# Performance work log

Hardware: AMD Instinct MI355X
Metric: run time of the kernel (lower is better)

Reference implementation:

```python
import jax, jax.numpy as jnp
import numpy as np

N_NODES = 100000
N_EDGES = 1600000
K = 3  # TAGConv default hops


def _make_lin(key, out_dim, in_dim):
    # K+1 bias-free linears (stacked) + one shared output bias, per PyG TAGConv
    kw, = jax.random.split(key, 1)
    scale = 1.0 / np.sqrt(in_dim)
    W = jax.random.uniform(kw, (K + 1, out_dim, in_dim), jnp.float32, -scale, scale)
    b = jnp.zeros((out_dim,), jnp.float32)
    return W, b


def setup_inputs() -> dict:
    key = jax.random.key(0)
    ks = jax.random.split(key, 6)
    x = jax.random.normal(ks[0], (N_NODES, 128), jnp.float32)
    edge_index = jax.random.randint(ks[1], (2, N_EDGES), 0, N_NODES, jnp.int64)
    W1, b1 = _make_lin(ks[2], 128, 128)
    W2, b2 = _make_lin(ks[3], 64, 128)
    W3, b3 = _make_lin(ks[4], 16, 64)
    return {"x": x, "edge_index": edge_index, "W1": W1, "b1": b1,
            "W2": W2, "b2": b2, "W3": W3, "b3": b3}


def _tagconv(x, row, col, norm, W, b, n):
    # out = sum_k lin_k(A_norm^k x) + b ; message x_j*norm gathered at col
    out = jnp.einsum('nd,od->no', x, W[0])
    h = x
    for k in range(1, W.shape[0]):
        h = jax.ops.segment_sum(norm[:, None] * h[row], col, num_segments=n)
        out = out + jnp.einsum('nd,od->no', h, W[k])
    return out + b


def _dropout(x, key, p=0.5):
    keep = jax.random.bernoulli(key, 1.0 - p, x.shape)
    return jnp.where(keep, x / (1.0 - p), 0.0)


def reference(x, edge_index, W1, b1, W2, b2, W3, b3):
    n = x.shape[0]
    row, col = edge_index[0], edge_index[1]
    # gcn_norm without self-loops (TAGConv default)
    deg = jax.ops.segment_sum(jnp.ones(row.shape[0], x.dtype), col, num_segments=n)
    dis = jnp.where(deg > 0, 1.0 / jnp.sqrt(jnp.where(deg > 0, deg, 1.0)), 0.0)
    norm = dis[row] * dis[col]

    dk1, dk2 = jax.random.split(jax.random.key(42))
    h = _tagconv(x, row, col, norm, W1, b1, n)
    h = _dropout(h, dk1)
    h = _tagconv(h, row, col, norm, W2, b2, n)
    h = jax.nn.elu(h)
    h = _dropout(h, dk2)
    h = _tagconv(h, row, col, norm, W3, b3, n)
    return h
```

## Files before the change

### kernel.cpp

```cpp
#include <hip/hip_runtime.h>
#include <stdint.h>
#include <math.h>

#define N_NODES 100000
#define N_EDGES 1600000

typedef __bf16 bf16_t;
typedef __attribute__((ext_vector_type(4))) __bf16 bf16x4;
typedef __attribute__((ext_vector_type(8))) __bf16 bf16x8;
typedef __attribute__((ext_vector_type(4))) float f32x4;

__device__ __forceinline__ f32x4 mfma16(bf16x8 a, bf16x8 b, f32x4 c) {
  return __builtin_amdgcn_mfma_f32_16x16x32_bf16(a, b, c, 0, 0, 0);
}

__device__ __host__ __forceinline__ uint32_t rotl32(uint32_t v, int d) {
  return (v << d) | (v >> (32 - d));
}

__device__ __host__ __forceinline__ void threefry2x32(uint32_t k0, uint32_t k1,
                                                      uint32_t x0, uint32_t x1,
                                                      uint32_t& o0, uint32_t& o1) {
  uint32_t ks0 = k0, ks1 = k1, ks2 = k0 ^ k1 ^ 0x1BD11BDAu;
  x0 += ks0; x1 += ks1;
#define TF_R(r) { x0 += x1; x1 = rotl32(x1, r); x1 ^= x0; }
  TF_R(13) TF_R(15) TF_R(26) TF_R(6)
  x0 += ks1; x1 += ks2 + 1u;
  TF_R(17) TF_R(29) TF_R(16) TF_R(24)
  x0 += ks2; x1 += ks0 + 2u;
  TF_R(13) TF_R(15) TF_R(26) TF_R(6)
  x0 += ks0; x1 += ks1 + 3u;
  TF_R(17) TF_R(29) TF_R(16) TF_R(24)
  x0 += ks1; x1 += ks2 + 4u;
  TF_R(13) TF_R(15) TF_R(26) TF_R(6)
  x0 += ks2; x1 += ks0 + 5u;
#undef TF_R
  o0 = x0; o1 = x1;
}

__device__ __forceinline__ float drop_scale(uint32_t idx, uint32_t k0, uint32_t k1) {
  uint32_t o0, o1;
  threefry2x32(k0, k1, 0u, idx, o0, o1);
  uint32_t bits = o0 ^ o1;
  float u = __uint_as_float((bits >> 9) | 0x3f800000u) - 1.0f;
  return (u < 0.5f) ? 2.0f : 0.0f;
}

__global__ __launch_bounds__(256) void detect_kernel(const int* __restrict__ ei,
                                                     int* __restrict__ found_nonzero) {
  int idx = blockIdx.x * 256 + threadIdx.x;
  size_t j = (size_t)idx * 781;
  if (ei[2 * j + 1] != 0) atomicOr(found_nonzero, 1);
}

__device__ __forceinline__ int edge_row(const int* ei, bool i32, int e) {
  return i32 ? ei[e] : ei[2 * (size_t)e];
}
__device__ __forceinline__ int edge_col(const int* ei, bool i32, int e) {
  return i32 ? ei[N_EDGES + e] : ei[2 * ((size_t)N_EDGES + (size_t)e)];
}

#define BKT_SHIFT 8
#define NBKT 391
#define BKT_CAP 6144
#define EPB 8192
#define NBLK 196
#define SCAN_M (NBKT * NBLK)

__global__ __launch_bounds__(256) void hist_kernel(const int* __restrict__ ei,
                                                   const int* __restrict__ flag,
                                                   int* __restrict__ hist) {
  __shared__ int h[NBKT];
  const int t = threadIdx.x, blk = blockIdx.x;
  for (int i = t; i < NBKT; i += 256) h[i] = 0;
  __syncthreads();
  const bool i32 = *flag != 0;
  const int e0 = blk * EPB;
  for (int i = t; i < EPB; i += 256) {
    int e = e0 + i;
    if (e < N_EDGES) atomicAdd(&h[edge_col(ei, i32, e) >> BKT_SHIFT], 1);
  }
  __syncthreads();
  for (int i = t; i < NBKT; i += 256) hist[i * NBLK + blk] = h[i];
}

__global__ __launch_bounds__(256) void btot_kernel(const int* __restrict__ hist,
                                                   int* __restrict__ btot) {
  __shared__ int sh[256];
  const int b = blockIdx.x, t = threadIdx.x;
  int s = 0;
  for (int i = t; i < NBLK; i += 256) s += hist[b * NBLK + i];
  sh[t] = s;
  __syncthreads();
  for (int ofs = 128; ofs > 0; ofs >>= 1) {
    if (t < ofs) sh[t] += sh[t + ofs];
    __syncthreads();
  }
  if (t == 0) btot[b] = sh[0];
}

__global__ __launch_bounds__(512) void bbase_kernel(const int* __restrict__ btot,
                                                    int* __restrict__ bbase,
                                                    int* __restrict__ S) {
  __shared__ int sh[512];
  const int t = threadIdx.x;
  int v = (t < NBKT) ? btot[t] : 0;
  sh[t] = v;
  __syncthreads();
  for (int ofs = 1; ofs < 512; ofs <<= 1) {
    int u = (t >= ofs) ? sh[t - ofs] : 0;
    __syncthreads();
    sh[t] += u;
    __syncthreads();
  }
  if (t < NBKT) bbase[t] = sh[t] - v;
  if (t == 0) S[SCAN_M] = N_EDGES;
}

__global__ __launch_bounds__(256) void bscan2_kernel(const int* __restrict__ hist,
                                                     const int* __restrict__ bbase,
                                                     int* __restrict__ S) {
  __shared__ int sh[256];
  const int b = blockIdx.x, t = threadIdx.x;
  int v = (t < NBLK) ? hist[b * NBLK + t] : 0;
  sh[t] = v;
  __syncthreads();
  for (int ofs = 1; ofs < 256; ofs <<= 1) {
    int u = (t >= ofs) ? sh[t - ofs] : 0;
    __syncthreads();
    sh[t] += u;
    __syncthreads();
  }
  if (t < NBLK) S[b * NBLK + t] = bbase[b] + sh[t] - v;
}

__global__ __launch_bounds__(256) void binfill_kernel(const int* __restrict__ ei,
                                                      const int* __restrict__ flag,
                                                      const int* __restrict__ S,
                                                      int2* __restrict__ bins) {
  __shared__ int cur[NBKT];
  const int t = threadIdx.x, blk = blockIdx.x;
  for (int i = t; i < NBKT; i += 256) cur[i] = S[i * NBLK + blk];
  __syncthreads();
  const bool i32 = *flag != 0;
  const int e0 = blk * EPB;
  for (int i = t; i < EPB; i += 256) {
    int e = e0 + i;
    if (e < N_EDGES) {
      int r = edge_row(ei, i32, e);
      int c = edge_col(ei, i32, e);
      int p = atomicAdd(&cur[c >> BKT_SHIFT], 1);
      bins[p] = make_int2(r, c);
    }
  }
}

__global__ __launch_bounds__(512) void degdis_scatter_kernel(
    const int2* __restrict__ bins, const int* __restrict__ S,
    float* __restrict__ dis, int* __restrict__ rptr,
    uint32_t* __restrict__ erow) {
  __shared__ int h[256];
  __shared__ int sc[256];
  __shared__ int loff[256];
  __shared__ int lcur[256];
  __shared__ uint32_t reord[BKT_CAP];
  const int b = blockIdx.x, t = threadIdx.x;
  const int Bb = S[b * NBLK];
  const int Be = S[(b + 1) * NBLK];
  const int cnt = min(Be - Bb, BKT_CAP);
  if (t < 256) h[t] = 0;
  __syncthreads();
  for (int i = t; i < cnt; i += 512)
    atomicAdd(&h[bins[Bb + i].y & 255], 1);
  __syncthreads();
  if (t < 256) sc[t] = h[t];
  __syncthreads();
  for (int ofs = 1; ofs < 256; ofs <<= 1) {
    int u = 0;
    if (t >= ofs && t < 256) u = sc[t - ofs];
    __syncthreads();
    if (t < 256) sc[t] += u;
    __syncthreads();
  }
  const int c0 = b << BKT_SHIFT;
  if (t < 256) {
    loff[t] = sc[t] - h[t];
    lcur[t] = 0;
    if (c0 + t < N_NODES) {
      int d = h[t];
      dis[c0 + t] = (d > 0) ? (1.0f / sqrtf((float)d)) : 0.0f;
      rptr[c0 + t] = Bb + sc[t] - d;
    }
  }
  if (b == NBKT - 1 && t == 0) rptr[N_NODES] = N_EDGES;
  __syncthreads();
  for (int i = t; i < cnt; i += 512) {
    int2 rec = bins[Bb + i];
    int lc = rec.y & 255;
    int p = atomicAdd(&lcur[lc], 1);
    reord[loff[lc] + p] = (uint32_t)rec.x;
  }
  __syncthreads();
  for (int i = t; i < cnt; i += 512) erow[Bb + i] = reord[i];
}

__global__ __launch_bounds__(256) void wcvt_kernel(
    const float* __restrict__ W1, const float* __restrict__ W2,
    const float* __restrict__ W3,
    bf16_t* __restrict__ Wb1, bf16_t* __restrict__ Wb2,
    bf16_t* __restrict__ Wb3) {
  int i = blockIdx.x * 256 + threadIdx.x;
  if (i < 65536) Wb1[i] = (bf16_t)W1[i];
  if (i < 32768) Wb2[i] = (bf16_t)W2[i];
  if (i < 4096)  Wb3[i] = (bf16_t)W3[i];
}

template <int DIN, int LOG_DOUT, int NCH, bool YB, bool AHL>
__global__ __launch_bounds__(256) void matmul_mfma_kernel(
    const void* __restrict__ hA, const void* __restrict__ hAlo,
    const bf16_t* __restrict__ Wb, const float* __restrict__ bias,
    float* __restrict__ y0, void* __restrict__ y1,
    void* __restrict__ y2, void* __restrict__ y3) {
  constexpr int LDK = DIN + 8;
  constexpr int DOUT = 1 << LOG_DOUT;
  constexpr int KI = DIN / 32;
  __shared__ bf16_t sm[2][64 * LDK];
  const int m0 = blockIdx.x * 64;
  const int tid = threadIdx.x;

  if (AHL) {
    constexpr int NL = 64 * DIN / 8 / 256;
#pragma unroll
    for (int it = 0; it < NL; ++it) {
      int idx = tid + it * 256;
      int r = idx / (DIN / 8), cc = (idx % (DIN / 8)) * 8;
      int gm = m0 + r;
      uint4 vh = make_uint4(0, 0, 0, 0), vl = make_uint4(0, 0, 0, 0);
      if (gm < N_NODES) {
        vh = ((const uint4*)hA)[((size_t)gm * DIN + cc) >> 3];
        vl = ((const uint4*)hAlo)[((size_t)gm * DIN + cc) >> 3];
      }
      *(uint4*)&sm[0][r * LDK + cc] = vh;
      *(uint4*)&sm[1][r * LDK + cc] = vl;
    }
  } else {
    constexpr int NL = 64 * DIN / 4 / 256;
    union U4 { bf16_t b[4]; uint2 u; };
#pragma unroll
    for (int it = 0; it < NL; ++it) {
      int idx = tid + it * 256;
      int r = idx / (DIN / 4), cc = (idx % (DIN / 4)) * 4;
      int gm = m0 + r;
      float4 v = (gm < N_NODES) ? ((const float4*)hA)[((size_t)gm * DIN + cc) >> 2]
                                : make_float4(0.f, 0.f, 0.f, 0.f);
      U4 hi, lo;
      hi.b[0] = (bf16_t)v.x; lo.b[0] = (bf16_t)(v.x - (float)hi.b[0]);
      hi.b[1] = (bf16_t)v.y; lo.b[1] = (bf16_t)(v.y - (float)hi.b[1]);
      hi.b[2] = (bf16_t)v.z; lo.b[2] = (bf16_t)(v.z - (float)hi.b[2]);
      hi.b[3] = (bf16_t)v.w; lo.b[3] = (bf16_t)(v.w - (float)hi.b[3]);
      *(uint2*)&sm[0][r * LDK + cc] = hi.u;
      *(uint2*)&sm[1][r * LDK + cc] = lo.u;
    }
  }
  __syncthreads();

  const int w = tid >> 6, lane = tid & 63;
  const int wm = w & 1, wn = w >> 1;
  const int quad = lane >> 4, lr = lane & 15;

  bf16x8 aH[2][KI], aL[2][KI];
#pragma unroll
  for (int mt = 0; mt < 2; ++mt)
#pragma unroll
    for (int ki = 0; ki < KI; ++ki) {
      int rowa = wm * 32 + mt * 16 + lr;
      int koff = ki * 32 + quad * 8;
      aH[mt][ki] = *(const bf16x8*)&sm[0][rowa * LDK + koff];
      aL[mt][ki] = *(const bf16x8*)&sm[1][rowa * LDK + koff];
    }
  __syncthreads();

  constexpr int NLB = 64 * DIN / 8 / 256;
  uint4 wreg[NLB];
#pragma unroll
  for (int it = 0; it < NLB; ++it) {
    int idx = tid + it * 256;
    int r = idx / (DIN / 8), cc = (idx % (DIN / 8)) * 8;
    wreg[it] = ((const uint4*)Wb)[(((size_t)r) * DIN + cc) >> 3];
    *(uint4*)&sm[0][r * LDK + cc] = wreg[it];
  }
  __syncthreads();

  for (int nc = 0; nc < NCH; ++nc) {
    int p = nc & 1;
    if (nc + 1 < NCH) {
#pragma unroll
      for (int it = 0; it < NLB; ++it) {
        int idx = tid + it * 256;
        int r = idx / (DIN / 8), cc = (idx % (DIN / 8)) * 8;
        wreg[it] = ((const uint4*)Wb)[(((size_t)((nc + 1) * 64 + r)) * DIN + cc) >> 3];
      }
    }

    f32x4 acc[2][2] = {};
#pragma unroll
    for (int ki = 0; ki < KI; ++ki) {
      int koff = ki * 32 + quad * 8;
      bf16x8 bfr[2];
#pragma unroll
      for (int nt = 0; nt < 2; ++nt)
        bfr[nt] = *(const bf16x8*)&sm[p][(wn * 32 + nt * 16 + lr) * LDK + koff];
#pragma unroll
      for (int mt = 0; mt < 2; ++mt)
#pragma unroll
        for (int nt = 0; nt < 2; ++nt) {
          acc[mt][nt] = mfma16(bfr[nt], aH[mt][ki], acc[mt][nt]);
          acc[mt][nt] = mfma16(bfr[nt], aL[mt][ki], acc[mt][nt]);
        }
    }

    if (nc + 1 < NCH) {
#pragma unroll
      for (int it = 0; it < NLB; ++it) {
        int idx = tid + it * 256;
        int r = idx / (DIN / 8), cc = (idx % (DIN / 8)) * 8;
        *(uint4*)&sm[p ^ 1][r * LDK + cc] = wreg[it];
      }
    }
    __syncthreads();

    const int n0 = nc * 64;
#pragma unroll
    for (int mt = 0; mt < 2; ++mt) {
      int m = m0 + wm * 32 + mt * 16 + lr;
      if (m >= N_NODES) continue;
#pragma unroll
      for (int nt = 0; nt < 2; ++nt) {
        int nb = n0 + wn * 32 + nt * 16 + quad * 4;
        int k = nb >> LOG_DOUT;
        int o = nb & (DOUT - 1);
        size_t oi = (size_t)m * DOUT + o;
        if (k == 0) {
          float4 bv = *(const float4*)&bias[o];
          float4 st = make_float4(acc[mt][nt][0] + bv.x, acc[mt][nt][1] + bv.y,
                                  acc[mt][nt][2] + bv.z, acc[mt][nt][3] + bv.w);
          *(float4*)&y0[oi] = st;
        } else {
          void* yk = (k == 1) ? y1 : (k == 2) ? y2 : y3;
          if (YB) {
            bf16x4 bb;
            bb.x = (bf16_t)acc[mt][nt][0];
            bb.y = (bf16_t)acc[mt][nt][1];
            bb.z = (bf16_t)acc[mt][nt][2];
            bb.w = (bf16_t)acc[mt][nt][3];
            *(bf16x4*)((bf16_t*)yk + oi) = bb;
          } else {
            *(f32x4*)((float*)yk + oi) = acc[mt][nt];
          }
        }
      }
    }
  }
}

template <int D, int EPI, bool ABF, int OMODE>
__global__ __launch_bounds__(256) void prop_kernel(
    const bf16_t* __restrict__ zv, const void* __restrict__ addv,
    void* __restrict__ outv, void* __restrict__ outv2,
    const int* __restrict__ rptr, const uint32_t* __restrict__ erow,
    const float* __restrict__ dis, uint32_t k0, uint32_t k1) {
  constexpr int LPN = D / 4;
  constexpr int NPB = 256 / LPN;
  const int lane = threadIdx.x % LPN;
  const int nsub = threadIdx.x / LPN;
  const int c = blockIdx.x * NPB + nsub;
  if (c >= N_NODES) return;
  const int e0 = rptr[c], e1 = rptr[c + 1];
  const float dc = dis[c];
  const bf16x4* zs = (const bf16x4*)zv;
  float a0 = 0.f, a1 = 0.f, a2 = 0.f, a3 = 0.f;

  int e = e0;
  for (; e + 7 < e1; e += 8) {
    uint32_t r8[8];
#pragma unroll
    for (int j = 0; j < 8; ++j) r8[j] = erow[e + j];
    float w8[8];
    bf16x4 v8[8];
#pragma unroll
    for (int j = 0; j < 8; ++j) {
      w8[j] = dis[r8[j]];
      v8[j] = zs[(size_t)r8[j] * LPN + lane];
    }
#pragma unroll
    for (int j = 0; j < 8; ++j) {
      float w = w8[j] * dc;
      a0 = fmaf(w, (float)v8[j].x, a0);
      a1 = fmaf(w, (float)v8[j].y, a1);
      a2 = fmaf(w, (float)v8[j].z, a2);
      a3 = fmaf(w, (float)v8[j].w, a3);
    }
  }
  if (e + 3 < e1) {
    uint32_t r4[4];
#pragma unroll
    for (int j = 0; j < 4; ++j) r4[j] = erow[e + j];
    float w4[4];
    bf16x4 v4[4];
#pragma unroll
    for (int j = 0; j < 4; ++j) {
      w4[j] = dis[r4[j]];
      v4[j] = zs[(size_t)r4[j] * LPN + lane];
    }
#pragma unroll
    for (int j = 0; j < 4; ++j) {
      float w = w4[j] * dc;
      a0 = fmaf(w, (float)v4[j].x, a0);
      a1 = fmaf(w, (float)v4[j].y, a1);
      a2 = fmaf(w, (float)v4[j].z, a2);
      a3 = fmaf(w, (float)v4[j].w, a3);
    }
    e += 4;
  }
  for (; e < e1; ++e) {
    uint32_t r = erow[e];
    float w = dis[r] * dc;
    bf16x4 t = zs[(size_t)r * LPN + lane];
    a0 = fmaf(w, (float)t.x, a0);
    a1 = fmaf(w, (float)t.y, a1);
    a2 = fmaf(w, (float)t.z, a2);
    a3 = fmaf(w, (float)t.w, a3);
  }

  const size_t pidx = (size_t)c * LPN + lane;
  const uint32_t fidx = (uint32_t)c * D + 4 * lane;
  float ax[4];
  if (ABF) {
    bf16x4 t = ((const bf16x4*)addv)[pidx];
    ax[0] = (float)t.x; ax[1] = (float)t.y; ax[2] = (float)t.z; ax[3] = (float)t.w;
  } else {
    float4 t = ((const float4*)addv)[pidx];
    ax[0] = t.x; ax[1] = t.y; ax[2] = t.z; ax[3] = t.w;
  }
  float o[4] = {a0 + ax[0], a1 + ax[1], a2 + ax[2], a3 + ax[3]};
  if (EPI == 1) {
#pragma unroll
    for (int j = 0; j < 4; ++j) o[j] *= drop_scale(fidx + j, k0, k1);
  }
  if (EPI == 2) {
#pragma unroll
    for (int j = 0; j < 4; ++j) {
      o[j] = (o[j] > 0.f) ? o[j] : expm1f(o[j]);
      o[j] *= drop_scale(fidx + j, k0, k1);
    }
  }
  if (OMODE == 0) {
    ((float4*)outv)[pidx] = make_float4(o[0], o[1], o[2], o[3]);
  } else if (OMODE == 1) {
    bf16x4 bv;
    bv.x = (bf16_t)o[0]; bv.y = (bf16_t)o[1];
    bv.z = (bf16_t)o[2]; bv.w = (bf16_t)o[3];
    ((bf16x4*)outv)[pidx] = bv;
  } else {
    bf16x4 hv, lv;
    hv.x = (bf16_t)o[0]; hv.y = (bf16_t)o[1];
    hv.z = (bf16_t)o[2]; hv.w = (bf16_t)o[3];
    lv.x = (bf16_t)(o[0] - (float)hv.x);
    lv.y = (bf16_t)(o[1] - (float)hv.y);
    lv.z = (bf16_t)(o[2] - (float)hv.z);
    lv.w = (bf16_t)(o[3] - (float)hv.w);
    ((bf16x4*)outv)[pidx] = hv;
    ((bf16x4*)outv2)[pidx] = lv;
  }
}

extern "C" void kernel_launch(void* const* d_in, const int* in_sizes, int n_in,
                              void* d_out, int out_size, void* d_ws, size_t ws_size,
                              hipStream_t stream) {
  const float* x  = (const float*)d_in[0];
  const int*   ei = (const int*)d_in[1];
  const float* W1 = (const float*)d_in[2];
  const float* b1 = (const float*)d_in[3];
  const float* W2 = (const float*)d_in[4];
  const float* b2 = (const float*)d_in[5];
  const float* W3 = (const float*)d_in[6];
  const float* b3 = (const float*)d_in[7];
  float* out = (float*)d_out;

  char* ws = (char*)d_ws;
  size_t off = 0;
  auto alloc = [&](size_t bytes) -> char* {
    char* p = ws + off;
    off += (bytes + 255) & ~(size_t)255;
    return p;
  };
  int*   flag   = (int*)alloc(256);
  float* dis    = (float*)alloc((size_t)N_NODES * 4);
  int*   rptr   = (int*)alloc((size_t)(N_NODES + 1) * 4);
  int*   hist   = (int*)alloc((size_t)SCAN_M * 4);
  int*   S      = (int*)alloc((size_t)(SCAN_M + 1) * 4);
  int*   btot   = (int*)alloc((size_t)NBKT * 4);
  int*   bbase  = (int*)alloc((size_t)NBKT * 4);
  uint32_t* erow = (uint32_t*)alloc((size_t)N_EDGES * 4);
  bf16_t* Wb1  = (bf16_t*)alloc(65536 * 2);
  bf16_t* Wb2  = (bf16_t*)alloc(32768 * 2);
  bf16_t* Wb3  = (bf16_t*)alloc(4096 * 2);
  float*  R0  = (float*)alloc((size_t)N_NODES * 128 * 4);
  float*  R2  = (float*)alloc((size_t)N_NODES * 16 * 4);
  bf16_t* Zb0 = (bf16_t*)alloc((size_t)N_NODES * 128 * 2);
  bf16_t* Zb1 = (bf16_t*)alloc((size_t)N_NODES * 128 * 2);
  bf16_t* Bb1 = (bf16_t*)alloc((size_t)N_NODES * 128 * 2);
  bf16_t* Bb2 = (bf16_t*)alloc((size_t)N_NODES * 128 * 2);

  int2* bins = (int2*)R0;

  hipMemsetAsync(flag, 0, 256, stream);

  detect_kernel<<<8, 256, 0, stream>>>(ei, flag);
  hist_kernel<<<NBLK, 256, 0, stream>>>(ei, flag, hist);
  btot_kernel<<<NBKT, 256, 0, stream>>>(hist, btot);
  bbase_kernel<<<1, 512, 0, stream>>>(btot, bbase, S);
  bscan2_kernel<<<NBKT, 256, 0, stream>>>(hist, bbase, S);
  binfill_kernel<<<NBLK, 256, 0, stream>>>(ei, flag, S, bins);
  degdis_scatter_kernel<<<NBKT, 512, 0, stream>>>(bins, S, dis, rptr, erow);
  wcvt_kernel<<<256, 256, 0, stream>>>(W1, W2, W3, Wb1, Wb2, Wb3);

  uint32_t d10, d11, d20, d21;
  threefry2x32(0u, 42u, 0u, 0u, d10, d11);
  threefry2x32(0u, 42u, 0u, 1u, d20, d21);

  const int MB = (N_NODES + 63) / 64;
  const int PB128 = (N_NODES + 7) / 8;
  const int PB64n = (N_NODES + 15) / 16;
  const int PB16n = (N_NODES + 63) / 64;

  matmul_mfma_kernel<128, 7, 8, true, false><<<MB, 256, 0, stream>>>(
      x, nullptr, Wb1, b1, R0, Bb1, Bb2, Zb0);
  prop_kernel<128, 0, true, 1><<<PB128, 256, 0, stream>>>(
      Zb0, Bb2, Zb1, nullptr, rptr, erow, dis, 0, 0);
  prop_kernel<128, 0, true, 1><<<PB128, 256, 0, stream>>>(
      Zb1, Bb1, Zb0, nullptr, rptr, erow, dis, 0, 0);
  prop_kernel<128, 1, false, 2><<<PB128, 256, 0, stream>>>(
      Zb0, R0, Bb2, Bb1, rptr, erow, dis, d10, d11);

  float*  R1f = R0;
  bf16_t* S0 = Zb0;
  bf16_t* S1 = Zb0 + (size_t)N_NODES * 64;
  bf16_t* S2 = Zb1;
  bf16_t* S3 = Zb1 + (size_t)N_NODES * 64;
  matmul_mfma_kernel<128, 6, 4, true, true><<<MB, 256, 0, stream>>>(
      Bb2, Bb1, Wb2, b2, R1f, S2, S3, S0);
  prop_kernel<64, 0, true, 1><<<PB64n, 256, 0, stream>>>(
      S0, S3, S1, nullptr, rptr, erow, dis, 0, 0);
  prop_kernel<64, 0, true, 1><<<PB64n, 256, 0, stream>>>(
      S1, S2, S0, nullptr, rptr, erow, dis, 0, 0);
  prop_kernel<64, 2, false, 2><<<PB64n, 256, 0, stream>>>(
      S0, R1f, S2, S3, rptr, erow, dis, d20, d21);

  float*  z0f = R2;
  bf16_t* zb1 = Bb1;
  bf16_t* zb2 = Bb1 + (size_t)N_NODES * 16;
  bf16_t* zb3 = Bb1 + (size_t)N_NODES * 32;
  matmul_mfma_kernel<64, 4, 1, true, true><<<MB, 256, 0, stream>>>(
      S2, S3, Wb3, b3, z0f, zb1, zb2, zb3);
  prop_kernel<16, 0, true, 1><<<PB16n, 256, 0, stream>>>(
      zb3, zb2, zb2, nullptr, rptr, erow, dis, 0, 0);
  prop_kernel<16, 0, true, 1><<<PB16n, 256, 0, stream>>>(
      zb2, zb1, zb1, nullptr, rptr, erow, dis, 0, 0);
  prop_kernel<16, 0, false, 0><<<PB16n, 256, 0, stream>>>(
      zb1, z0f, out, nullptr, rptr, erow, dis, 0, 0);

  (void)in_sizes; (void)n_in; (void)out_size; (void)ws_size;
}
```

Measured before the change: 648.8 us.

## Widen prop lanes to 8 bf16 and degree-sort nodes within buckets

The propagation kernel now gives each lane 8 bf16 features through 16-byte loads instead of 4, halving lanes per node and doubling nodes per block. The CSR build also adds a per-bucket counting sort of nodes by in-degree, and prop blocks walk nodes in that order so nodes of similar degree share a wavefront. This targets load-instruction count and divergence in wavefronts that mix high- and low-degree nodes. It costs an extra index indirection and a small scan in the scatter kernel, and each thread now keeps more registers live.

Result: slower. 726.5 us (+12.0%).

```diff
diff --git a/kernel.cpp b/kernel.cpp
--- a/kernel.cpp
+++ b/kernel.cpp
@@ -158,11 +158,13 @@
 __global__ __launch_bounds__(512) void degdis_scatter_kernel(
     const int2* __restrict__ bins, const int* __restrict__ S,
     float* __restrict__ dis, int* __restrict__ rptr,
-    uint32_t* __restrict__ erow) {
+    uint32_t* __restrict__ erow, int* __restrict__ nord) {
   __shared__ int h[256];
   __shared__ int sc[256];
   __shared__ int loff[256];
   __shared__ int lcur[256];
+  __shared__ int dh[64];
+  __shared__ int dcur[64];
   __shared__ uint32_t reord[BKT_CAP];
   const int b = blockIdx.x, t = threadIdx.x;
   const int Bb = S[b * NBLK];
@@ -183,16 +185,36 @@
     __syncthreads();
   }
   const int c0 = b << BKT_SHIFT;
+  const int nn = min(256, N_NODES - c0);
   if (t < 256) {
     loff[t] = sc[t] - h[t];
     lcur[t] = 0;
-    if (c0 + t < N_NODES) {
+    if (t < nn) {
       int d = h[t];
       dis[c0 + t] = (d > 0) ? (1.0f / sqrtf((float)d)) : 0.0f;
       rptr[c0 + t] = Bb + sc[t] - d;
     }
   }
   if (b == NBKT - 1 && t == 0) rptr[N_NODES] = N_EDGES;
+  if (t < 64) dh[t] = 0;
+  __syncthreads();
+  if (t < nn) atomicAdd(&dh[min(h[t], 63)], 1);
+  __syncthreads();
+  if (t < 64) dcur[t] = dh[t];
+  __syncthreads();
+  for (int ofs = 1; ofs < 64; ofs <<= 1) {
+    int u = 0;
+    if (t >= ofs && t < 64) u = dcur[t - ofs];
+    __syncthreads();
+    if (t < 64) dcur[t] += u;
+    __syncthreads();
+  }
+  if (t < 64) dcur[t] -= dh[t];
+  __syncthreads();
+  if (t < nn) {
+    int pos = atomicAdd(&dcur[min(h[t], 63)], 1);
+    nord[c0 + pos] = c0 + t;
+  }
   __syncthreads();
   for (int i = t; i < cnt; i += 512) {
     int2 rec = bins[Bb + i];
@@ -368,17 +390,19 @@
     const bf16_t* __restrict__ zv, const void* __restrict__ addv,
     void* __restrict__ outv, void* __restrict__ outv2,
     const int* __restrict__ rptr, const uint32_t* __restrict__ erow,
-    const float* __restrict__ dis, uint32_t k0, uint32_t k1) {
-  constexpr int LPN = D / 4;
+    const float* __restrict__ dis, const int* __restrict__ nord,
+    uint32_t k0, uint32_t k1) {
+  constexpr int LPN = D / 8;
   constexpr int NPB = 256 / LPN;
   const int lane = threadIdx.x % LPN;
   const int nsub = threadIdx.x / LPN;
-  const int c = blockIdx.x * NPB + nsub;
-  if (c >= N_NODES) return;
+  const int ci = blockIdx.x * NPB + nsub;
+  if (ci >= N_NODES) return;
+  const int c = nord[ci];
   const int e0 = rptr[c], e1 = rptr[c + 1];
   const float dc = dis[c];
-  const bf16x4* zs = (const bf16x4*)zv;
-  float a0 = 0.f, a1 = 0.f, a2 = 0.f, a3 = 0.f;
+  const bf16x8* zs = (const bf16x8*)zv;
+  float a[8] = {};
 
   int e = e0;
   for (; e + 7 < e1; e += 8) {
@@ -386,7 +410,7 @@
 #pragma unroll
     for (int j = 0; j < 8; ++j) r8[j] = erow[e + j];
     float w8[8];
-    bf16x4 v8[8];
+    bf16x8 v8[8];
 #pragma unroll
     for (int j = 0; j < 8; ++j) {
       w8[j] = dis[r8[j]];
@@ -395,10 +419,8 @@
 #pragma unroll
     for (int j = 0; j < 8; ++j) {
       float w = w8[j] * dc;
-      a0 = fmaf(w, (float)v8[j].x, a0);
-      a1 = fmaf(w, (float)v8[j].y, a1);
-      a2 = fmaf(w, (float)v8[j].z, a2);
-      a3 = fmaf(w, (float)v8[j].w, a3);
+#pragma unroll
+      for (int q = 0; q < 8; ++q) a[q] = fmaf(w, (float)v8[j][q], a[q]);
     }
   }
   if (e + 3 < e1) {
@@ -406,7 +428,7 @@
 #pragma unroll
     for (int j = 0; j < 4; ++j) r4[j] = erow[e + j];
     float w4[4];
-    bf16x4 v4[4];
+    bf16x8 v4[4];
 #pragma unroll
     for (int j = 0; j < 4; ++j) {
       w4[j] = dis[r4[j]];
@@ -415,62 +437,62 @@
 #pragma unroll
     for (int j = 0; j < 4; ++j) {
       float w = w4[j] * dc;
-      a0 = fmaf(w, (float)v4[j].x, a0);
-      a1 = fmaf(w, (float)v4[j].y, a1);
-      a2 = fmaf(w, (float)v4[j].z, a2);
-      a3 = fmaf(w, (float)v4[j].w, a3);
+#pragma unroll
+      for (int q = 0; q < 8; ++q) a[q] = fmaf(w, (float)v4[j][q], a[q]);
     }
     e += 4;
   }
   for (; e < e1; ++e) {
     uint32_t r = erow[e];
     float w = dis[r] * dc;
-    bf16x4 t = zs[(size_t)r * LPN + lane];
-    a0 = fmaf(w, (float)t.x, a0);
-    a1 = fmaf(w, (float)t.y, a1);
-    a2 = fmaf(w, (float)t.z, a2);
-    a3 = fmaf(w, (float)t.w, a3);
+    bf16x8 t = zs[(size_t)r * LPN + lane];
+#pragma unroll
+    for (int q = 0; q < 8; ++q) a[q] = fmaf(w, (float)t[q], a[q]);
   }
 
   const size_t pidx = (size_t)c * LPN + lane;
-  const uint32_t fidx = (uint32_t)c * D + 4 * lane;
-  float ax[4];
+  const size_t fidx4 = ((size_t)c * D + lane * 8) >> 2;
+  const uint32_t fidx = (uint32_t)c * D + (uint32_t)(lane * 8);
+  float o[8];
   if (ABF) {
-    bf16x4 t = ((const bf16x4*)addv)[pidx];
-    ax[0] = (float)t.x; ax[1] = (float)t.y; ax[2] = (float)t.z; ax[3] = (float)t.w;
+    bf16x8 t = ((const bf16x8*)addv)[pidx];
+#pragma unroll
+    for (int q = 0; q < 8; ++q) o[q] = a[q] + (float)t[q];
   } else {
-    float4 t = ((const float4*)addv)[pidx];
-    ax[0] = t.x; ax[1] = t.y; ax[2] = t.z; ax[3] = t.w;
-  }
-  float o[4] = {a0 + ax[0], a1 + ax[1], a2 + ax[2], a3 + ax[3]};
+    const float4* af = (const float4*)addv;
+    float4 t0 = af[fidx4], t1 = af[fidx4 + 1];
+    o[0] = a[0] + t0.x; o[1] = a[1] + t0.y; o[2] = a[2] + t0.z; o[3] = a[3] + t0.w;
+    o[4] = a[4] + t1.x; o[5] = a[5] + t1.y; o[6] = a[6] + t1.z; o[7] = a[7] + t1.w;
+  }
   if (EPI == 1) {
 #pragma unroll
-    for (int j = 0; j < 4; ++j) o[j] *= drop_scale(fidx + j, k0, k1);
+    for (int q = 0; q < 8; ++q) o[q] *= drop_scale(fidx + q, k0, k1);
   }
   if (EPI == 2) {
 #pragma unroll
-    for (int j = 0; j < 4; ++j) {
-      o[j] = (o[j] > 0.f) ? o[j] : expm1f(o[j]);
-      o[j] *= drop_scale(fidx + j, k0, k1);
+    for (int q = 0; q < 8; ++q) {
+      o[q] = (o[q] > 0.f) ? o[q] : expm1f(o[q]);
+      o[q] *= drop_scale(fidx + q, k0, k1);
     }
   }
   if (OMODE == 0) {
-    ((float4*)outv)[pidx] = make_float4(o[0], o[1], o[2], o[3]);
+    float4* of = (float4*)outv;
+    of[fidx4] = make_float4(o[0], o[1], o[2], o[3]);
+    of[fidx4 + 1] = make_float4(o[4], o[5], o[6], o[7]);
   } else if (OMODE == 1) {
-    bf16x4 bv;
-    bv.x = (bf16_t)o[0]; bv.y = (bf16_t)o[1];
-    bv.z = (bf16_t)o[2]; bv.w = (bf16_t)o[3];
-    ((bf16x4*)outv)[pidx] = bv;
+    bf16x8 bv;
+#pragma unroll
+    for (int q = 0; q < 8; ++q) bv[q] = (bf16_t)o[q];
+    ((bf16x8*)outv)[pidx] = bv;
   } else {
-    bf16x4 hv, lv;
-    hv.x = (bf16_t)o[0]; hv.y = (bf16_t)o[1];
-    hv.z = (bf16_t)o[2]; hv.w = (bf16_t)o[3];
-    lv.x = (bf16_t)(o[0] - (float)hv.x);
-    lv.y = (bf16_t)(o[1] - (float)hv.y);
-    lv.z = (bf16_t)(o[2] - (float)hv.z);
-    lv.w = (bf16_t)(o[3] - (float)hv.w);
-    ((bf16x4*)outv)[pidx] = hv;
-    ((bf16x4*)outv2)[pidx] = lv;
+    bf16x8 hv, lv;
+#pragma unroll
+    for (int q = 0; q < 8; ++q) {
+      hv[q] = (bf16_t)o[q];
+      lv[q] = (bf16_t)(o[q] - (float)hv[q]);
+    }
+    ((bf16x8*)outv)[pidx] = hv;
+    ((bf16x8*)outv2)[pidx] = lv;
   }
 }
 
@@ -497,6 +519,7 @@
   int*   flag   = (int*)alloc(256);
   float* dis    = (float*)alloc((size_t)N_NODES * 4);
   int*   rptr   = (int*)alloc((size_t)(N_NODES + 1) * 4);
+  int*   nord   = (int*)alloc((size_t)N_NODES * 4);
   int*   hist   = (int*)alloc((size_t)SCAN_M * 4);
   int*   S      = (int*)alloc((size_t)(SCAN_M + 1) * 4);
   int*   btot   = (int*)alloc((size_t)NBKT * 4);
@@ -522,7 +545,7 @@
   bbase_kernel<<<1, 512, 0, stream>>>(btot, bbase, S);
   bscan2_kernel<<<NBKT, 256, 0, stream>>>(hist, bbase, S);
   binfill_kernel<<<NBLK, 256, 0, stream>>>(ei, flag, S, bins);
-  degdis_scatter_kernel<<<NBKT, 512, 0, stream>>>(bins, S, dis, rptr, erow);
+  degdis_scatter_kernel<<<NBKT, 512, 0, stream>>>(bins, S, dis, rptr, erow, nord);
   wcvt_kernel<<<256, 256, 0, stream>>>(W1, W2, W3, Wb1, Wb2, Wb3);
 
   uint32_t d10, d11, d20, d21;
@@ -530,18 +553,18 @@
   threefry2x32(0u, 42u, 0u, 1u, d20, d21);
 
   const int MB = (N_NODES + 63) / 64;
-  const int PB128 = (N_NODES + 7) / 8;
-  const int PB64n = (N_NODES + 15) / 16;
-  const int PB16n = (N_NODES + 63) / 64;
+  const int PB128 = (N_NODES + 15) / 16;
+  const int PB64n = (N_NODES + 31) / 32;
+  const int PB16n = (N_NODES + 127) / 128;
 
   matmul_mfma_kernel<128, 7, 8, true, false><<<MB, 256, 0, stream>>>(
       x, nullptr, Wb1, b1, R0, Bb1, Bb2, Zb0);
   prop_kernel<128, 0, true, 1><<<PB128, 256, 0, stream>>>(
-      Zb0, Bb2, Zb1, nullptr, rptr, erow, dis, 0, 0);
+      Zb0, Bb2, Zb1, nullptr, rptr, erow, dis, nord, 0, 0);
   prop_kernel<128, 0, true, 1><<<PB128, 256, 0, stream>>>(
-      Zb1, Bb1, Zb0, nullptr, rptr, erow, dis, 0, 0);
+      Zb1, Bb1, Zb0, nullptr, rptr, erow, dis, nord, 0, 0);
   prop_kernel<128, 1, false, 2><<<PB128, 256, 0, stream>>>(
-      Zb0, R0, Bb2, Bb1, rptr, erow, dis, d10, d11);
+      Zb0, R0, Bb2, Bb1, rptr, erow, dis, nord, d10, d11);
 
   float*  R1f = R0;
   bf16_t* S0 = Zb0;
@@ -551,11 +574,11 @@
   matmul_mfma_kernel<128, 6, 4, true, true><<<MB, 256, 0, stream>>>(
       Bb2, Bb1, Wb2, b2, R1f, S2, S3, S0);
   prop_kernel<64, 0, true, 1><<<PB64n, 256, 0, stream>>>(
-      S0, S3, S1, nullptr, rptr, erow, dis, 0, 0);
+      S0, S3, S1, nullptr, rptr, erow, dis, nord, 0, 0);
   prop_kernel<64, 0, true, 1><<<PB64n, 256, 0, stream>>>(
-      S1, S2, S0, nullptr, rptr, erow, dis, 0, 0);
+      S1, S2, S0, nullptr, rptr, erow, dis, nord, 0, 0);
   prop_kernel<64, 2, false, 2><<<PB64n, 256, 0, stream>>>(
-      S0, R1f, S2, S3, rptr, erow, dis, d20, d21);
+      S0, R1f, S2, S3, rptr, erow, dis, nord, d20, d21);
 
   float*  z0f = R2;
   bf16_t* zb1 = Bb1;
@@ -564,11 +587,11 @@
   matmul_mfma_kernel<64, 4, 1, true, true><<<MB, 256, 0, stream>>>(
       S2, S3, Wb3, b3, z0f, zb1, zb2, zb3);
   prop_kernel<16, 0, true, 1><<<PB16n, 256, 0, stream>>>(
-      zb3, zb2, zb2, nullptr, rptr, erow, dis, 0, 0);
+      zb3, zb2, zb2, nullptr, rptr, erow, dis, nord, 0, 0);
   prop_kernel<16, 0, true, 1><<<PB16n, 256, 0, stream>>>(
-      zb2, zb1, zb1, nullptr, rptr, erow, dis, 0, 0);
+      zb2, zb1, zb1, nullptr, rptr, erow, dis, nord, 0, 0);
   prop_kernel<16, 0, false, 0><<<PB16n, 256, 0, stream>>>(
-      zb1, z0f, out, nullptr, rptr, erow, dis, 0, 0);
+      zb1, z0f, out, nullptr, rptr, erow, dis, nord, 0, 0);
 
   (void)in_sizes; (void)n_in; (void)out_size; (void)ws_size;
 }
```
